# Performance work log

Measured on AMD Instinct MI355X. Metric: run time of the kernel, lower is better.

The kernel has to match this reference:

```python
import jax, jax.numpy as jnp
import numpy as np

D_MODEL = 512
D_FF = 2048
N_EXPERTS = 8
TOP_K = 2
AUX_COEF = 0.01
Z_COEF = 1e-4
N_LAYERS = 12
INIT_STD = 0.02


def setup_inputs() -> dict:
    key = jax.random.key(0)
    kx, kr, k1, k2, k3 = jax.random.split(key, 5)
    std2 = INIT_STD / np.sqrt(2 * N_LAYERS)  # scale_init_by_depth for w2
    x = jax.random.normal(kx, (4, 1024, D_MODEL), dtype=jnp.float32)
    router_w = jax.random.normal(kr, (D_MODEL, N_EXPERTS), dtype=jnp.float32) * 0.02
    w1 = jax.random.normal(k1, (N_EXPERTS, D_MODEL, D_FF), dtype=jnp.float32) * INIT_STD
    w2 = jax.random.normal(k2, (N_EXPERTS, D_FF, D_MODEL), dtype=jnp.float32) * std2
    w3 = jax.random.normal(k3, (N_EXPERTS, D_MODEL, D_FF), dtype=jnp.float32) * INIT_STD
    return {"x": x, "router_w": router_w, "w1": w1, "w2": w2, "w3": w3}


def reference(x, router_w, w1, w2, w3):
    B, S, D = x.shape
    xf = x.reshape(-1, D)                              # [N, D]
    n_tokens = xf.shape[0]

    router_logits = xf @ router_w                      # [N, E]
    probs = jax.nn.softmax(router_logits.astype(jnp.float32), axis=-1)
    topk_w, topk_i = jax.lax.top_k(probs, TOP_K)       # [N, K]
    topk_w = topk_w / jnp.sum(topk_w, axis=-1, keepdims=True)

    # combine weight per (token, expert): zero for non-selected experts
    combine = jnp.sum(jax.nn.one_hot(topk_i, N_EXPERTS, dtype=jnp.float32)
                      * topk_w[..., None], axis=1)     # [N, E]

    # SwiGLU per expert, masked combine (same math as sorted grouped GEMM + scatter-add)
    gate = jax.nn.silu(jnp.einsum('nd,edf->enf', xf, w1))   # [E, N, F]
    up = jnp.einsum('nd,edf->enf', xf, w3)                  # [E, N, F]
    expert_out = jnp.einsum('enf,efd->end', gate * up, w2)  # [E, N, D]
    out = jnp.einsum('end,ne->nd', expert_out, combine.astype(x.dtype))

    # losses
    importance = probs.mean(axis=0)                    # [E]
    load = jax.nn.one_hot(topk_i[:, 0], N_EXPERTS, dtype=jnp.float32).mean(axis=0)
    aux_loss = N_EXPERTS * jnp.sum(importance * load) * AUX_COEF
    z_loss = jnp.mean(router_logits.astype(jnp.float32) ** 2) * Z_COEF

    return out.reshape(B, S, D), aux_loss, z_loss
```

## Files before the change

kernel.cpp:

```cpp
#include <hip/hip_runtime.h>
#include <hip/hip_fp16.h>

#define D_MODEL 512
#define D_FF    2048
#define NEXP    8
#define NTOK    4096
#define NPAIR   8192
#define DUMMY   NPAIR
#define LSTRIDE 4224
#define MAXTILES 72
#define WBSTR   (4096 * 512)

typedef _Float16 half8  __attribute__((ext_vector_type(8)));
typedef _Float16 half2v __attribute__((ext_vector_type(2)));
typedef float    f32x4  __attribute__((ext_vector_type(4)));

__device__ __forceinline__ void gload16(const void* g, void* l) {
  __builtin_amdgcn_global_load_lds(
      (const __attribute__((address_space(1))) unsigned*)g,
      (__attribute__((address_space(3))) unsigned*)l, 16, 0, 0);
}

#define PIPE_BARRIER(N) do { \
  asm volatile("s_waitcnt vmcnt(" #N ")" ::: "memory"); \
  __builtin_amdgcn_s_barrier(); \
  asm volatile("" ::: "memory"); \
} while (0)

__global__ __launch_bounds__(256) void k_prep(
    const float* __restrict__ x, const float* __restrict__ rw,
    const float* __restrict__ w1, const float* __restrict__ w3,
    const float* __restrict__ w2, _Float16* __restrict__ wB,
    _Float16* __restrict__ w2t, _Float16* __restrict__ xb,
    int* __restrict__ topE, float* __restrict__ wcomb,
    float* __restrict__ blk, int* __restrict__ ntiles) {
  __shared__ float t[64][65];
  int tid = threadIdx.x;
  if (blockIdx.x < 6144) {
    int bt = blockIdx.x;
    const float* src; int rb, cb, e; bool isw3 = false, isw2 = (bt >= 4096);
    if (!isw2) {
      isw3 = (bt >= 2048);
      src = isw3 ? w3 : w1;
      int tt = bt & 2047; e = tt >> 8; int rem = tt & 255;
      rb = (rem >> 5) * 64; cb = (rem & 31) * 64;
      src += (size_t)e * D_MODEL * D_FF;
    } else {
      int tt = bt - 4096; e = tt >> 8; int rem = tt & 255;
      src = w2;
      rb = (rem >> 3) * 64; cb = (rem & 7) * 64;
      src += (size_t)e * D_FF * D_MODEL;
    }
    int C = isw2 ? D_MODEL : D_FF;
    int tx = tid & 15, ty = tid >> 4;
#pragma unroll
    for (int i = 0; i < 4; i++) {
      float4 v = *(const float4*)(src + (size_t)(rb + ty + i * 16) * C + cb + tx * 4);
      t[ty + i * 16][tx * 4 + 0] = v.x;
      t[ty + i * 16][tx * 4 + 1] = v.y;
      t[ty + i * 16][tx * 4 + 2] = v.z;
      t[ty + i * 16][tx * 4 + 3] = v.w;
    }
    __syncthreads();
    int tx2 = tid & 31, ty2 = tid >> 5;
#pragma unroll
    for (int i = 0; i < 8; i++) {
      int c = ty2 + i * 8;
      int r = tx2 * 2;
      half2v p = {(_Float16)t[r][c], (_Float16)t[r + 1][c]};
      if (!isw2) {
        int f = cb + c;
        int j = ((f >> 5) << 6) + (isw3 ? 32 : 0) + (f & 31);
        *(half2v*)(wB + (size_t)e * WBSTR + (size_t)j * D_MODEL + rb + r) = p;
      } else {
        *(half2v*)(w2t + (size_t)e * D_MODEL * D_FF + (size_t)(cb + c) * D_FF + rb + r) = p;
      }
    }
  } else {
    int bx = blockIdx.x - 6144;
    __shared__ float s_imp[NEXP];
    __shared__ float s_z;
    if (tid < NEXP) s_imp[tid] = 0.f;
    if (tid == 0) s_z = 0.f;
    if (bx == 0 && tid == 0) ntiles[0] = 0;
    __syncthreads();
    int wave = tid >> 6, lane = tid & 63;
    int n = bx * 4 + wave;
    const float* xr = x + (size_t)n * D_MODEL;
    float acc[8] = {0, 0, 0, 0, 0, 0, 0, 0};
    float4 v0 = *(const float4*)(xr + lane * 8);
    float4 v1 = *(const float4*)(xr + lane * 8 + 4);
    float xs[8] = {v0.x, v0.y, v0.z, v0.w, v1.x, v1.y, v1.z, v1.w};
    half8 hx = {(_Float16)xs[0], (_Float16)xs[1], (_Float16)xs[2], (_Float16)xs[3],
                (_Float16)xs[4], (_Float16)xs[5], (_Float16)xs[6], (_Float16)xs[7]};
    *(half8*)(xb + (size_t)n * D_MODEL + lane * 8) = hx;
#pragma unroll
    for (int j = 0; j < 8; j++) {
      const float4* w4 = (const float4*)(rw + (size_t)(lane * 8 + j) * NEXP);
      float4 wa = w4[0], wb = w4[1];
      acc[0] += xs[j] * wa.x; acc[1] += xs[j] * wa.y;
      acc[2] += xs[j] * wa.z; acc[3] += xs[j] * wa.w;
      acc[4] += xs[j] * wb.x; acc[5] += xs[j] * wb.y;
      acc[6] += xs[j] * wb.z; acc[7] += xs[j] * wb.w;
    }
#pragma unroll
    for (int off = 32; off >= 1; off >>= 1) {
#pragma unroll
      for (int e = 0; e < 8; e++) acc[e] += __shfl_xor(acc[e], off);
    }
    if (lane == 0) {
      float z = 0.f;
#pragma unroll
      for (int e = 0; e < 8; e++) z += acc[e] * acc[e];
      float m = acc[0];
#pragma unroll
      for (int e = 1; e < 8; e++) m = fmaxf(m, acc[e]);
      float p[8], s = 0.f;
#pragma unroll
      for (int e = 0; e < 8; e++) { p[e] = expf(acc[e] - m); s += p[e]; }
      float inv = 1.f / s;
#pragma unroll
      for (int e = 0; e < 8; e++) p[e] *= inv;
      int e0 = 0; float p0 = p[0];
#pragma unroll
      for (int e = 1; e < 8; e++) if (p[e] > p0) { p0 = p[e]; e0 = e; }
      int e1 = -1; float p1 = -1.f;
#pragma unroll
      for (int e = 0; e < 8; e++) if (e != e0 && p[e] > p1) { p1 = p[e]; e1 = e; }
      float wsum = p0 + p1;
      topE[n] = e0 | (e1 << 4);
      wcomb[2 * n] = p0 / wsum;
      wcomb[2 * n + 1] = p1 / wsum;
#pragma unroll
      for (int e = 0; e < 8; e++) atomicAdd(&s_imp[e], p[e]);
      atomicAdd(&s_z, z);
    }
    __syncthreads();
    if (tid < 8) blk[bx * 9 + tid] = s_imp[tid];
    if (tid == 8) blk[bx * 9 + 8] = s_z;
  }
}

__global__ __launch_bounds__(1024) void k_scatter(
    const int* __restrict__ topE, int* __restrict__ lists,
    int* __restrict__ tiletab, int* __restrict__ ntiles,
    int* __restrict__ loadc_g) {
  int e = blockIdx.x;
  __shared__ int wcount[16];
  __shared__ int lcw[16];
  __shared__ int sbase;
  __shared__ int stot;
  int tid = threadIdx.x, lane = tid & 63, wv = tid >> 6;
  if (lane == 0) lcw[wv] = 0;
  int total = 0;
  for (int c = 0; c < 8; c++) {
    int idx = c * 1024 + tid;
    int te = topE[idx >> 1];
    int ee = (idx & 1) ? ((te >> 4) & 15) : (te & 15);
    bool mine = (ee == e);
    unsigned long long bal = __ballot(mine);
    unsigned long long balL = __ballot(mine && !(idx & 1));
    int rank = __popcll(bal & ((1ull << lane) - 1ull));
    if (lane == 0) {
      wcount[wv] = __popcll(bal);
      lcw[wv] += __popcll(balL);
    }
    __syncthreads();
    int pre = total;
    for (int w2 = 0; w2 < wv; w2++) pre += wcount[w2];
    if (mine) lists[e * LSTRIDE + pre + rank] = idx;
    int t16 = 0;
#pragma unroll
    for (int w2 = 0; w2 < 16; w2++) t16 += wcount[w2];
    __syncthreads();
    total += t16;
  }
  int tiles = (total + 127) >> 7;
  if (tid == 0) {
    int lc = 0;
#pragma unroll
    for (int w2 = 0; w2 < 16; w2++) lc += lcw[w2];
    loadc_g[e] = lc;
    sbase = atomicAdd(ntiles, tiles);
    stot = total;
  }
  __syncthreads();
  if (tid < tiles) tiletab[sbase + tid] = e | (tid << 8);
  if (tid < 128) {
    int p = stot + tid;
    if (p < tiles * 128) lists[e * LSTRIDE + p] = DUMMY;
  }
}

__global__ __launch_bounds__(1024) void k_losses(
    const float* __restrict__ blk, const int* __restrict__ loadc_g,
    float* __restrict__ out) {
  __shared__ float fin[9];
  int tid = threadIdx.x, lane = tid & 63, wv = tid >> 6;
  if (wv < 9) {
    float s = 0.f;
    for (int b = lane; b < 1024; b += 64) s += blk[b * 9 + wv];
#pragma unroll
    for (int off = 32; off >= 1; off >>= 1) s += __shfl_xor(s, off);
    if (lane == 0) fin[wv] = s;
  }
  __syncthreads();
  if (tid == 0) {
    float a = 0.f;
#pragma unroll
    for (int e = 0; e < 8; e++)
      a += (fin[e] * (1.f / 4096.f)) * ((float)loadc_g[e] * (1.f / 4096.f));
    out[NTOK * D_MODEL] = 8.f * a * 0.01f;
    out[NTOK * D_MODEL + 1] = fin[8] * (1.f / (4096.f * 8.f)) * 1e-4f;
  }
}

__global__ __launch_bounds__(512) void k_gemm1(
    const _Float16* __restrict__ xb, const _Float16* __restrict__ wB,
    _Float16* __restrict__ h, const int* __restrict__ lists,
    const int* __restrict__ tiletab, const int* __restrict__ ntiles) {
  int ti = blockIdx.y;
  if (ti >= ntiles[0]) return;
  int ent = tiletab[ti];
  int e = ent & 15, mt = ent >> 8, nt = blockIdx.x;
  __shared__ __align__(16) _Float16 Asl[2][128 * 64];
  __shared__ __align__(16) _Float16 Bsl[2][256 * 64];
  __shared__ int toks[128];
  int tid = threadIdx.x, lane = tid & 63, w = tid >> 6;
  if (tid < 128) toks[tid] = lists[e * LSTRIDE + mt * 128 + tid];
  __syncthreads();
  const _Float16* wBe = wB + (size_t)e * WBSTR;
  int l3 = lane >> 3, l7 = lane & 7;
  const _Float16* aSrc[2];
  const _Float16* bSrc[4];
#pragma unroll
  for (int g = 0; g < 2; g++) {
    int r = w * 16 + g * 8 + l3;
    aSrc[g] = xb + (size_t)(toks[r] >> 1) * D_MODEL + ((l7 ^ (r & 7)) << 3);
  }
#pragma unroll
  for (int g = 0; g < 4; g++) {
    int r = w * 32 + g * 8 + l3;
    bSrc[g] = wBe + (size_t)(nt * 256 + r) * D_MODEL + ((l7 ^ (r & 7)) << 3);
  }
  int wm = w >> 2, wn = w & 3;
  int la = lane & 15, lh = lane >> 4;
  int aoff[4][2], boff[4][2];
#pragma unroll
  for (int mf = 0; mf < 4; mf++)
#pragma unroll
    for (int kh = 0; kh < 2; kh++) {
      int r = wm * 64 + mf * 16 + la;
      aoff[mf][kh] = r * 64 + (((kh * 4 + lh) ^ (r & 7)) << 3);
      int rb = wn * 64 + mf * 16 + la;
      boff[mf][kh] = rb * 64 + (((kh * 4 + lh) ^ (rb & 7)) << 3);
    }
  f32x4 acc[4][4] = {};
#pragma unroll
  for (int g = 0; g < 2; g++) gload16(aSrc[g], &Asl[0][(w * 16 + g * 8) * 64]);
#pragma unroll
  for (int g = 0; g < 4; g++) gload16(bSrc[g], &Bsl[0][(w * 32 + g * 8) * 64]);
  PIPE_BARRIER(0);
#pragma unroll
  for (int t = 0; t < 8; t++) {
    const int cur = t & 1, nb = cur ^ 1;
    const int k1 = (t + 1) * 64;
    if (t < 7) {
#pragma unroll
      for (int g = 0; g < 2; g++) gload16(aSrc[g] + k1, &Asl[nb][(w * 16 + g * 8) * 64]);
    }
    half8 af[4], bf[4];
#pragma unroll
    for (int nf = 0; nf < 4; nf++) bf[nf] = *(const half8*)(&Bsl[cur][boff[nf][0]]);
#pragma unroll
    for (int mf = 0; mf < 4; mf++) af[mf] = *(const half8*)(&Asl[cur][aoff[mf][0]]);
#pragma unroll
    for (int mf = 0; mf < 4; mf++)
#pragma unroll
      for (int nf = 0; nf < 4; nf++)
        acc[mf][nf] = __builtin_amdgcn_mfma_f32_16x16x32_f16(af[mf], bf[nf], acc[mf][nf], 0, 0, 0);
    if (t < 7) {
#pragma unroll
      for (int g = 0; g < 4; g++) gload16(bSrc[g] + k1, &Bsl[nb][(w * 32 + g * 8) * 64]);
    }
#pragma unroll
    for (int nf = 0; nf < 4; nf++) bf[nf] = *(const half8*)(&Bsl[cur][boff[nf][1]]);
#pragma unroll
    for (int mf = 0; mf < 4; mf++) af[mf] = *(const half8*)(&Asl[cur][aoff[mf][1]]);
#pragma unroll
    for (int mf = 0; mf < 4; mf++)
#pragma unroll
      for (int nf = 0; nf < 4; nf++)
        acc[mf][nf] = __builtin_amdgcn_mfma_f32_16x16x32_f16(af[mf], bf[nf], acc[mf][nf], 0, 0, 0);
    PIPE_BARRIER(0);
  }
  int fbase = (nt * 4 + wn) * 32;
#pragma unroll
  for (int mf = 0; mf < 4; mf++) {
    int mb = wm * 64 + mf * 16 + (lh << 2);
#pragma unroll
    for (int q = 0; q < 4; q++) {
      int m = mb + q;
      int pair = toks[m];
      _Float16* hrow = h + (size_t)pair * D_FF + fbase;
#pragma unroll
      for (int nf = 0; nf < 2; nf++) {
        float g = acc[mf][nf][q], u = acc[mf][nf + 2][q];
        hrow[nf * 16 + la] = (_Float16)((g / (1.f + __expf(-g))) * u);
      }
    }
  }
}

__global__ __launch_bounds__(512) void k_gemm2(
    const _Float16* __restrict__ h, const _Float16* __restrict__ w2t,
    float* __restrict__ po2, const int* __restrict__ lists,
    const int* __restrict__ tiletab, const int* __restrict__ ntiles,
    const float* __restrict__ wcomb) {
  int ti = blockIdx.y;
  if (ti >= ntiles[0]) return;
  int ent = tiletab[ti];
  int e = ent & 15, mt = ent >> 8;
  int nt = blockIdx.x & 1, ks = blockIdx.x >> 1;
  __shared__ __align__(16) _Float16 Asl[2][128 * 64];
  __shared__ __align__(16) _Float16 Bsl[2][256 * 64];
  __shared__ int toks[128];
  __shared__ float wcs[128];
  int tid = threadIdx.x, lane = tid & 63, w = tid >> 6;
  if (tid < 128) {
    int p = lists[e * LSTRIDE + mt * 128 + tid];
    toks[tid] = p;
    wcs[tid] = (p < NPAIR) ? wcomb[p] : 0.f;
  }
  __syncthreads();
  const _Float16* w2e = w2t + (size_t)e * D_MODEL * D_FF;
  const int kb = ks * 1024;
  int l3 = lane >> 3, l7 = lane & 7;
  const _Float16* aSrc[2];
  const _Float16* bSrc[4];
#pragma unroll
  for (int g = 0; g < 2; g++) {
    int r = w * 16 + g * 8 + l3;
    aSrc[g] = h + (size_t)toks[r] * D_FF + kb + ((l7 ^ (r & 7)) << 3);
  }
#pragma unroll
  for (int g = 0; g < 4; g++) {
    int r = w * 32 + g * 8 + l3;
    bSrc[g] = w2e + (size_t)(nt * 256 + r) * D_FF + kb + ((l7 ^ (r & 7)) << 3);
  }
  int wm = w >> 2, wn = w & 3;
  int la = lane & 15, lh = lane >> 4;
  int aoff[4][2], boff[4][2];
#pragma unroll
  for (int mf = 0; mf < 4; mf++)
#pragma unroll
    for (int kh = 0; kh < 2; kh++) {
      int r = wm * 64 + mf * 16 + la;
      aoff[mf][kh] = r * 64 + (((kh * 4 + lh) ^ (r & 7)) << 3);
      int rb = wn * 64 + mf * 16 + la;
      boff[mf][kh] = rb * 64 + (((kh * 4 + lh) ^ (rb & 7)) << 3);
    }
  f32x4 acc[4][4] = {};
#pragma unroll
  for (int g = 0; g < 2; g++) gload16(aSrc[g], &Asl[0][(w * 16 + g * 8) * 64]);
#pragma unroll
  for (int g = 0; g < 4; g++) gload16(bSrc[g], &Bsl[0][(w * 32 + g * 8) * 64]);
  PIPE_BARRIER(0);
#pragma unroll 2
  for (int t = 0; t < 16; t++) {
    const int cur = t & 1, nb = cur ^ 1;
    const int k1 = (t + 1) * 64;
    if (t < 15) {
#pragma unroll
      for (int g = 0; g < 2; g++) gload16(aSrc[g] + k1, &Asl[nb][(w * 16 + g * 8) * 64]);
    }
    half8 af[4], bf[4];
#pragma unroll
    for (int nf = 0; nf < 4; nf++) bf[nf] = *(const half8*)(&Bsl[cur][boff[nf][0]]);
#pragma unroll
    for (int mf = 0; mf < 4; mf++) af[mf] = *(const half8*)(&Asl[cur][aoff[mf][0]]);
#pragma unroll
    for (int mf = 0; mf < 4; mf++)
#pragma unroll
      for (int nf = 0; nf < 4; nf++)
        acc[mf][nf] = __builtin_amdgcn_mfma_f32_16x16x32_f16(af[mf], bf[nf], acc[mf][nf], 0, 0, 0);
    if (t < 15) {
#pragma unroll
      for (int g = 0; g < 4; g++) gload16(bSrc[g] + k1, &Bsl[nb][(w * 32 + g * 8) * 64]);
    }
#pragma unroll
    for (int nf = 0; nf < 4; nf++) bf[nf] = *(const half8*)(&Bsl[cur][boff[nf][1]]);
#pragma unroll
    for (int mf = 0; mf < 4; mf++) af[mf] = *(const half8*)(&Asl[cur][aoff[mf][1]]);
#pragma unroll
    for (int mf = 0; mf < 4; mf++)
#pragma unroll
      for (int nf = 0; nf < 4; nf++)
        acc[mf][nf] = __builtin_amdgcn_mfma_f32_16x16x32_f16(af[mf], bf[nf], acc[mf][nf], 0, 0, 0);
    PIPE_BARRIER(0);
  }
  int dbase = nt * 256 + wn * 64;
#pragma unroll
  for (int mf = 0; mf < 4; mf++) {
    int mb = wm * 64 + mf * 16 + (lh << 2);
#pragma unroll
    for (int q = 0; q < 4; q++) {
      int m = mb + q;
      int pair = toks[m];
      if (pair < NPAIR) {
        float wv = wcs[m];
        float* orow = po2 + ((size_t)ks * NPAIR + pair) * D_MODEL + dbase;
#pragma unroll
        for (int nf = 0; nf < 4; nf++)
          orow[nf * 16 + la] = acc[mf][nf][q] * wv;
      }
    }
  }
}

__global__ void k_combine(const float* __restrict__ po2, float* __restrict__ out) {
  int gid = blockIdx.x * blockDim.x + threadIdx.x;
  int r = gid >> 7;
  int c = (gid & 127) * 4;
  const float4 a0 = *(const float4*)(po2 + (size_t)(2 * r) * D_MODEL + c);
  const float4 a1 = *(const float4*)(po2 + (size_t)(2 * r + 1) * D_MODEL + c);
  const float4 b0 = *(const float4*)(po2 + (size_t)(NPAIR + 2 * r) * D_MODEL + c);
  const float4 b1 = *(const float4*)(po2 + (size_t)(NPAIR + 2 * r + 1) * D_MODEL + c);
  float4 o{a0.x + a1.x + b0.x + b1.x, a0.y + a1.y + b0.y + b1.y,
           a0.z + a1.z + b0.z + b1.z, a0.w + a1.w + b0.w + b1.w};
  *(float4*)(out + (size_t)r * D_MODEL + c) = o;
}

extern "C" void kernel_launch(void* const* d_in, const int* in_sizes, int n_in,
                              void* d_out, int out_size, void* d_ws, size_t ws_size,
                              hipStream_t stream) {
  const float* x = (const float*)d_in[0];
  const float* rw = (const float*)d_in[1];
  const float* w1 = (const float*)d_in[2];
  const float* w2 = (const float*)d_in[3];
  const float* w3 = (const float*)d_in[4];
  float* out = (float*)d_out;

  char* ws = (char*)d_ws;
  size_t o = 0;
  _Float16* wB = (_Float16*)(ws + o); o += (size_t)NEXP * WBSTR * 2;
  _Float16* w2t = (_Float16*)(ws + o); o += (size_t)NEXP * D_MODEL * D_FF * 2;
  _Float16* xb = (_Float16*)(ws + o); o += (size_t)(NTOK + 1) * D_MODEL * 2;
  _Float16* hbuf = (_Float16*)(ws + o); o += (size_t)(NPAIR + 1) * D_FF * 2;
  int* lists = (int*)(ws + o); o += (size_t)NEXP * LSTRIDE * 4;
  float* wcomb = (float*)(ws + o); o += (size_t)NPAIR * 4;
  int* topE = (int*)(ws + o); o += (size_t)NTOK * 4;
  float* blk = (float*)(ws + o); o += (size_t)1024 * 9 * 4;
  int* tiletab = (int*)(ws + o); o += MAXTILES * 4;
  int* ntiles = (int*)(ws + o); o += 16;
  int* loadc_g = (int*)(ws + o); o += 64;
  float* po2 = (float*)ws;
  if (ws_size < o) return;

  k_prep<<<7168, 256, 0, stream>>>(x, rw, w1, w3, w2, wB, w2t, xb, topE,
                                   wcomb, blk, ntiles);
  k_scatter<<<NEXP, 1024, 0, stream>>>(topE, lists, tiletab, ntiles, loadc_g);
  k_losses<<<1, 1024, 0, stream>>>(blk, loadc_g, out);
  k_gemm1<<<dim3(16, MAXTILES), 512, 0, stream>>>(xb, wB, hbuf, lists, tiletab, ntiles);
  k_gemm2<<<dim3(4, MAXTILES), 512, 0, stream>>>(hbuf, w2t, po2, lists, tiletab, ntiles, wcomb);
  k_combine<<<(NTOK * D_MODEL / 4 + 255) / 256, 256, 0, stream>>>(po2, out);
}
```

Measured before the change: 284.0 us.

## Triple-buffer expert GEMM pipelines with setprio and fold loss kernel into combine

Both grouped GEMM kernels move from a double-buffered LDS pipeline to a triple-buffered one. Loads run two k-steps ahead and partial vmcnt waits replace full drains, with s_setprio raised around the MFMA blocks. The separate single-block loss kernel is removed and its reduction now runs in block 0 of the combine kernel, saving one launch. LDS use per block grows from 96KB to 144KB, which may cut occupancy, and the extra barriers add sync overhead.

```diff
diff --git a/kernel.cpp b/kernel.cpp
--- a/kernel.cpp
+++ b/kernel.cpp
@@ -23,6 +23,11 @@
 
 #define PIPE_BARRIER(N) do { \
   asm volatile("s_waitcnt vmcnt(" #N ")" ::: "memory"); \
+  __builtin_amdgcn_s_barrier(); \
+  asm volatile("" ::: "memory"); \
+} while (0)
+#define BAR() do { \
+  asm volatile("" ::: "memory"); \
   __builtin_amdgcn_s_barrier(); \
   asm volatile("" ::: "memory"); \
 } while (0)
@@ -192,29 +197,6 @@
   }
 }
 
-__global__ __launch_bounds__(1024) void k_losses(
-    const float* __restrict__ blk, const int* __restrict__ loadc_g,
-    float* __restrict__ out) {
-  __shared__ float fin[9];
-  int tid = threadIdx.x, lane = tid & 63, wv = tid >> 6;
-  if (wv < 9) {
-    float s = 0.f;
-    for (int b = lane; b < 1024; b += 64) s += blk[b * 9 + wv];
-#pragma unroll
-    for (int off = 32; off >= 1; off >>= 1) s += __shfl_xor(s, off);
-    if (lane == 0) fin[wv] = s;
-  }
-  __syncthreads();
-  if (tid == 0) {
-    float a = 0.f;
-#pragma unroll
-    for (int e = 0; e < 8; e++)
-      a += (fin[e] * (1.f / 4096.f)) * ((float)loadc_g[e] * (1.f / 4096.f));
-    out[NTOK * D_MODEL] = 8.f * a * 0.01f;
-    out[NTOK * D_MODEL + 1] = fin[8] * (1.f / (4096.f * 8.f)) * 1e-4f;
-  }
-}
-
 __global__ __launch_bounds__(512) void k_gemm1(
     const _Float16* __restrict__ xb, const _Float16* __restrict__ wB,
     _Float16* __restrict__ h, const int* __restrict__ lists,
@@ -223,8 +205,8 @@
   if (ti >= ntiles[0]) return;
   int ent = tiletab[ti];
   int e = ent & 15, mt = ent >> 8, nt = blockIdx.x;
-  __shared__ __align__(16) _Float16 Asl[2][128 * 64];
-  __shared__ __align__(16) _Float16 Bsl[2][256 * 64];
+  __shared__ __align__(16) _Float16 Asl[3][128 * 64];
+  __shared__ __align__(16) _Float16 Bsl[3][256 * 64];
   __shared__ int toks[128];
   int tid = threadIdx.x, lane = tid & 63, w = tid >> 6;
   if (tid < 128) toks[tid] = lists[e * LSTRIDE + mt * 128 + tid];
@@ -256,44 +238,55 @@
       boff[mf][kh] = rb * 64 + (((kh * 4 + lh) ^ (rb & 7)) << 3);
     }
   f32x4 acc[4][4] = {};
-#pragma unroll
-  for (int g = 0; g < 2; g++) gload16(aSrc[g], &Asl[0][(w * 16 + g * 8) * 64]);
-#pragma unroll
-  for (int g = 0; g < 4; g++) gload16(bSrc[g], &Bsl[0][(w * 32 + g * 8) * 64]);
-  PIPE_BARRIER(0);
+#define G1_SA(T, BUF) do { _Pragma("unroll") \
+  for (int g = 0; g < 2; g++) gload16(aSrc[g] + (T) * 64, &Asl[BUF][(w * 16 + g * 8) * 64]); } while (0)
+#define G1_SB(T, BUF) do { _Pragma("unroll") \
+  for (int g = 0; g < 4; g++) gload16(bSrc[g] + (T) * 64, &Bsl[BUF][(w * 32 + g * 8) * 64]); } while (0)
+  G1_SA(0, 0); G1_SB(0, 0);
+  G1_SA(1, 1); G1_SB(1, 1);
+  PIPE_BARRIER(6);
 #pragma unroll
   for (int t = 0; t < 8; t++) {
-    const int cur = t & 1, nb = cur ^ 1;
-    const int k1 = (t + 1) * 64;
-    if (t < 7) {
-#pragma unroll
-      for (int g = 0; g < 2; g++) gload16(aSrc[g] + k1, &Asl[nb][(w * 16 + g * 8) * 64]);
-    }
-    half8 af[4], bf[4];
-#pragma unroll
-    for (int nf = 0; nf < 4; nf++) bf[nf] = *(const half8*)(&Bsl[cur][boff[nf][0]]);
-#pragma unroll
-    for (int mf = 0; mf < 4; mf++) af[mf] = *(const half8*)(&Asl[cur][aoff[mf][0]]);
-#pragma unroll
-    for (int mf = 0; mf < 4; mf++)
-#pragma unroll
-      for (int nf = 0; nf < 4; nf++)
-        acc[mf][nf] = __builtin_amdgcn_mfma_f32_16x16x32_f16(af[mf], bf[nf], acc[mf][nf], 0, 0, 0);
-    if (t < 7) {
-#pragma unroll
-      for (int g = 0; g < 4; g++) gload16(bSrc[g] + k1, &Bsl[nb][(w * 32 + g * 8) * 64]);
-    }
-#pragma unroll
-    for (int nf = 0; nf < 4; nf++) bf[nf] = *(const half8*)(&Bsl[cur][boff[nf][1]]);
-#pragma unroll
-    for (int mf = 0; mf < 4; mf++) af[mf] = *(const half8*)(&Asl[cur][aoff[mf][1]]);
-#pragma unroll
-    for (int mf = 0; mf < 4; mf++)
-#pragma unroll
-      for (int nf = 0; nf < 4; nf++)
-        acc[mf][nf] = __builtin_amdgcn_mfma_f32_16x16x32_f16(af[mf], bf[nf], acc[mf][nf], 0, 0, 0);
-    PIPE_BARRIER(0);
-  }
+    const int cur = t % 3, nxt = (t + 2) % 3;
+    {
+      half8 af[4], bf[4];
+#pragma unroll
+      for (int nf = 0; nf < 4; nf++) bf[nf] = *(const half8*)(&Bsl[cur][boff[nf][0]]);
+#pragma unroll
+      for (int mf = 0; mf < 4; mf++) af[mf] = *(const half8*)(&Asl[cur][aoff[mf][0]]);
+      if (t < 6) G1_SA(t + 2, nxt);
+      BAR();
+      __builtin_amdgcn_s_setprio(1);
+#pragma unroll
+      for (int mf = 0; mf < 4; mf++)
+#pragma unroll
+        for (int nf = 0; nf < 4; nf++)
+          acc[mf][nf] = __builtin_amdgcn_mfma_f32_16x16x32_f16(af[mf], bf[nf], acc[mf][nf], 0, 0, 0);
+      __builtin_amdgcn_s_setprio(0);
+      BAR();
+    }
+    {
+      half8 af[4], bf[4];
+#pragma unroll
+      for (int nf = 0; nf < 4; nf++) bf[nf] = *(const half8*)(&Bsl[cur][boff[nf][1]]);
+#pragma unroll
+      for (int mf = 0; mf < 4; mf++) af[mf] = *(const half8*)(&Asl[cur][aoff[mf][1]]);
+      if (t < 6) G1_SB(t + 2, nxt);
+      if (t < 6)      PIPE_BARRIER(6);
+      else if (t == 6) PIPE_BARRIER(0);
+      else            BAR();
+      __builtin_amdgcn_s_setprio(1);
+#pragma unroll
+      for (int mf = 0; mf < 4; mf++)
+#pragma unroll
+        for (int nf = 0; nf < 4; nf++)
+          acc[mf][nf] = __builtin_amdgcn_mfma_f32_16x16x32_f16(af[mf], bf[nf], acc[mf][nf], 0, 0, 0);
+      __builtin_amdgcn_s_setprio(0);
+      if (t < 7) BAR();
+    }
+  }
+#undef G1_SA
+#undef G1_SB
   int fbase = (nt * 4 + wn) * 32;
 #pragma unroll
   for (int mf = 0; mf < 4; mf++) {
@@ -322,8 +315,8 @@
   int ent = tiletab[ti];
   int e = ent & 15, mt = ent >> 8;
   int nt = blockIdx.x & 1, ks = blockIdx.x >> 1;
-  __shared__ __align__(16) _Float16 Asl[2][128 * 64];
-  __shared__ __align__(16) _Float16 Bsl[2][256 * 64];
+  __shared__ __align__(16) _Float16 Asl[3][128 * 64];
+  __shared__ __align__(16) _Float16 Bsl[3][256 * 64];
   __shared__ int toks[128];
   __shared__ float wcs[128];
   int tid = threadIdx.x, lane = tid & 63, w = tid >> 6;
@@ -361,44 +354,55 @@
       boff[mf][kh] = rb * 64 + (((kh * 4 + lh) ^ (rb & 7)) << 3);
     }
   f32x4 acc[4][4] = {};
-#pragma unroll
-  for (int g = 0; g < 2; g++) gload16(aSrc[g], &Asl[0][(w * 16 + g * 8) * 64]);
-#pragma unroll
-  for (int g = 0; g < 4; g++) gload16(bSrc[g], &Bsl[0][(w * 32 + g * 8) * 64]);
-  PIPE_BARRIER(0);
-#pragma unroll 2
+#define G2_SA(T, BUF) do { _Pragma("unroll") \
+  for (int g = 0; g < 2; g++) gload16(aSrc[g] + (T) * 64, &Asl[BUF][(w * 16 + g * 8) * 64]); } while (0)
+#define G2_SB(T, BUF) do { _Pragma("unroll") \
+  for (int g = 0; g < 4; g++) gload16(bSrc[g] + (T) * 64, &Bsl[BUF][(w * 32 + g * 8) * 64]); } while (0)
+  G2_SA(0, 0); G2_SB(0, 0);
+  G2_SA(1, 1); G2_SB(1, 1);
+  PIPE_BARRIER(6);
+#pragma unroll
   for (int t = 0; t < 16; t++) {
-    const int cur = t & 1, nb = cur ^ 1;
-    const int k1 = (t + 1) * 64;
-    if (t < 15) {
-#pragma unroll
-      for (int g = 0; g < 2; g++) gload16(aSrc[g] + k1, &Asl[nb][(w * 16 + g * 8) * 64]);
-    }
-    half8 af[4], bf[4];
-#pragma unroll
-    for (int nf = 0; nf < 4; nf++) bf[nf] = *(const half8*)(&Bsl[cur][boff[nf][0]]);
-#pragma unroll
-    for (int mf = 0; mf < 4; mf++) af[mf] = *(const half8*)(&Asl[cur][aoff[mf][0]]);
-#pragma unroll
-    for (int mf = 0; mf < 4; mf++)
-#pragma unroll
-      for (int nf = 0; nf < 4; nf++)
-        acc[mf][nf] = __builtin_amdgcn_mfma_f32_16x16x32_f16(af[mf], bf[nf], acc[mf][nf], 0, 0, 0);
-    if (t < 15) {
-#pragma unroll
-      for (int g = 0; g < 4; g++) gload16(bSrc[g] + k1, &Bsl[nb][(w * 32 + g * 8) * 64]);
-    }
-#pragma unroll
-    for (int nf = 0; nf < 4; nf++) bf[nf] = *(const half8*)(&Bsl[cur][boff[nf][1]]);
-#pragma unroll
-    for (int mf = 0; mf < 4; mf++) af[mf] = *(const half8*)(&Asl[cur][aoff[mf][1]]);
-#pragma unroll
-    for (int mf = 0; mf < 4; mf++)
-#pragma unroll
-      for (int nf = 0; nf < 4; nf++)
-        acc[mf][nf] = __builtin_amdgcn_mfma_f32_16x16x32_f16(af[mf], bf[nf], acc[mf][nf], 0, 0, 0);
-    PIPE_BARRIER(0);
-  }
+    const int cur = t % 3, nxt = (t + 2) % 3;
+    {
+      half8 af[4], bf[4];
+#pragma unroll
+      for (int nf = 0; nf < 4; nf++) bf[nf] = *(const half8*)(&Bsl[cur][boff[nf][0]]);
+#pragma unroll
+      for (int mf = 0; mf < 4; mf++) af[mf] = *(const half8*)(&Asl[cur][aoff[mf][0]]);
+      if (t < 14) G2_SA(t + 2, nxt);
+      BAR();
+      __builtin_amdgcn_s_setprio(1);
+#pragma unroll
+      for (int mf = 0; mf < 4; mf++)
+#pragma unroll
+        for (int nf = 0; nf < 4; nf++)
+          acc[mf][nf] = __builtin_amdgcn_mfma_f32_16x16x32_f16(af[mf], bf[nf], acc[mf][nf], 0, 0, 0);
+      __builtin_amdgcn_s_setprio(0);
+      BAR();
+    }
+    {
+      half8 af[4], bf[4];
+#pragma unroll
+      for (int nf = 0; nf < 4; nf++) bf[nf] = *(const half8*)(&Bsl[cur][boff[nf][1]]);
+#pragma unroll
+      for (int mf = 0; mf < 4; mf++) af[mf] = *(const half8*)(&Asl[cur][aoff[mf][1]]);
+      if (t < 14) G2_SB(t + 2, nxt);
+      if (t < 14)      PIPE_BARRIER(6);
+      else if (t == 14) PIPE_BARRIER(0);
+      else             BAR();
+      __builtin_amdgcn_s_setprio(1);
+#pragma unroll
+      for (int mf = 0; mf < 4; mf++)
+#pragma unroll
+        for (int nf = 0; nf < 4; nf++)
+          acc[mf][nf] = __builtin_amdgcn_mfma_f32_16x16x32_f16(af[mf], bf[nf], acc[mf][nf], 0, 0, 0);
+      __builtin_amdgcn_s_setprio(0);
+      if (t < 15) BAR();
+    }
+  }
+#undef G2_SA
+#undef G2_SB
   int dbase = nt * 256 + wn * 64;
 #pragma unroll
   for (int mf = 0; mf < 4; mf++) {
@@ -418,7 +422,9 @@
   }
 }
 
-__global__ void k_combine(const float* __restrict__ po2, float* __restrict__ out) {
+__global__ void k_combine(const float* __restrict__ po2, float* __restrict__ out,
+                          const float* __restrict__ blk,
+                          const int* __restrict__ loadc_g) {
   int gid = blockIdx.x * blockDim.x + threadIdx.x;
   int r = gid >> 7;
   int c = (gid & 127) * 4;
@@ -429,6 +435,26 @@
   float4 o{a0.x + a1.x + b0.x + b1.x, a0.y + a1.y + b0.y + b1.y,
            a0.z + a1.z + b0.z + b1.z, a0.w + a1.w + b0.w + b1.w};
   *(float4*)(out + (size_t)r * D_MODEL + c) = o;
+  if (blockIdx.x == 0) {
+    __shared__ float fin[9];
+    int lane = threadIdx.x & 63, wv = threadIdx.x >> 6;
+    for (int j = wv; j < 9; j += 4) {
+      float s = 0.f;
+      for (int b = lane; b < 1024; b += 64) s += blk[b * 9 + j];
+#pragma unroll
+      for (int off = 32; off >= 1; off >>= 1) s += __shfl_xor(s, off);
+      if (lane == 0) fin[j] = s;
+    }
+    __syncthreads();
+    if (threadIdx.x == 0) {
+      float a = 0.f;
+#pragma unroll
+      for (int e = 0; e < 8; e++)
+        a += (fin[e] * (1.f / 4096.f)) * ((float)loadc_g[e] * (1.f / 4096.f));
+      out[NTOK * D_MODEL] = 8.f * a * 0.01f;
+      out[NTOK * D_MODEL + 1] = fin[8] * (1.f / (4096.f * 8.f)) * 1e-4f;
+    }
+  }
 }
 
 extern "C" void kernel_launch(void* const* d_in, const int* in_sizes, int n_in,
@@ -460,8 +486,7 @@
   k_prep<<<7168, 256, 0, stream>>>(x, rw, w1, w3, w2, wB, w2t, xb, topE,
                                    wcomb, blk, ntiles);
   k_scatter<<<NEXP, 1024, 0, stream>>>(topE, lists, tiletab, ntiles, loadc_g);
-  k_losses<<<1, 1024, 0, stream>>>(blk, loadc_g, out);
   k_gemm1<<<dim3(16, MAXTILES), 512, 0, stream>>>(xb, wB, hbuf, lists, tiletab, ntiles);
   k_gemm2<<<dim3(4, MAXTILES), 512, 0, stream>>>(hbuf, w2t, po2, lists, tiletab, ntiles, wcomb);
-  k_combine<<<(NTOK * D_MODEL / 4 + 255) / 256, 256, 0, stream>>>(po2, out);
-}
+  k_combine<<<(NTOK * D_MODEL / 4 + 255) / 256, 256, 0, stream>>>(po2, out, blk, loadc_g);
+}
```

New measurement: 284.2 us. No clear change (+0.1%).
